# Optimization experiments

Hardware: AMD Instinct MI355X
Metric: run time of the kernel (lower is better)

Reference implementation:

```python
import jax, jax.numpy as jnp
import numpy as np


def fwht(x):
    """Fast Walsh-Hadamard transform along last axis (n must be a power of 2).
    Loop runs log2(n) times (fixed, ~12 iters) -- fully vectorized butterflies."""
    n = x.shape[-1]
    prefix = x.shape[:-1]
    x = x.reshape(-1, n)
    h = 1
    while h < n:
        x = x.reshape(-1, n // (2 * h), 2, h)
        a, b = x[:, :, 0, :], x[:, :, 1, :]
        x = jnp.stack([a + b, a - b], axis=2).reshape(-1, n)
        h *= 2
    return x.reshape(prefix + (n,))


def setup_inputs() -> dict:
    key = jax.random.key(0)
    ks = jax.random.split(key, 8)
    Bz, S, N, M = 4, 2048, 4096, 4096   # batch, seq, in_features, out_features
    CODESZ, CB_SIZE, RANK = 8, 256, 64
    inp = {}
    inp["input"] = jax.random.normal(ks[0], (Bz, S, N), dtype=jnp.float32)
    inp["Qidxs"] = jax.random.randint(ks[1], (M, N // CODESZ), 0, CB_SIZE, dtype=jnp.int32)
    inp["codebook_vals"] = jax.random.normal(ks[2], (CB_SIZE, CODESZ), dtype=jnp.float32)
    # SU/SV are random sign vectors in QuIP#
    inp["SU"] = jnp.sign(jax.random.normal(ks[3], (N,), dtype=jnp.float32))
    inp["SV"] = jnp.sign(jax.random.normal(ks[4], (M,), dtype=jnp.float32))
    inp["Wscale"] = jnp.ones((), dtype=jnp.float32)
    inp["A"] = jax.random.normal(ks[5], (M, RANK), dtype=jnp.float32) * 0.01
    inp["B"] = jax.random.normal(ks[6], (RANK, N), dtype=jnp.float32) * 0.01
    return inp


def reference(input, Qidxs, codebook_vals, SU, SV, Wscale, A, B):
    n = SU.shape[0]   # in_features
    m = SV.shape[0]   # out_features
    lead = input.shape[:-1]
    x = input.reshape(-1, n).astype(jnp.float32)          # [T, n]
    # input rotation: x <- H^T (x * SU) / sqrt(n)   (matmul_hadUt, K=1 case)
    x = fwht(x * SU) * (1.0 / jnp.sqrt(jnp.float32(n)))
    # low-rank correction branch (rank > 0)
    Bx = x @ B.T                                          # [T, rank]
    # dequantize: codebook lookup [m, n/codesz, codesz] -> [m, n]
    W = codebook_vals[Qidxs].reshape(m, n)
    z = (x @ W.T) * Wscale                                # [T, m]
    z = z + Bx @ A.T
    # output rotation: z <- SV * (H z) / sqrt(m)
    z = fwht(z) * (1.0 / jnp.sqrt(jnp.float32(m))) * SV
    return z.reshape(lead + (m,))
```

## Files before the change

### kernel.cpp

```cpp
#include <hip/hip_runtime.h>
#include <hip/hip_bf16.h>


typedef __attribute__((ext_vector_type(8))) short short8;
typedef __attribute__((ext_vector_type(4))) float f32x4;

#define T_ROWS 8192
#define NDIM   4096
#define MDIM   4096
#define NT     (NDIM / 64)

__device__ __forceinline__ void gld_lds16(const void* g, void* lds_uniform) {
    __builtin_amdgcn_global_load_lds(
        (const __attribute__((address_space(1))) unsigned int*)(unsigned long long)(uintptr_t)g,
        (__attribute__((address_space(3))) unsigned int*)(unsigned int)(uintptr_t)lds_uniform,
        16, 0, 0);
}

__device__ __forceinline__ void bfly(float& a, float& b) {
    float s = a + b, d = a - b; a = s; b = d;
}

__device__ __forceinline__ void fwht16(float* v) {
#pragma unroll
    for (int h = 1; h <= 8; h <<= 1)
#pragma unroll
        for (int j = 0; j < 16; ++j)
            if (!(j & h)) bfly(v[j], v[j | h]);
}

__global__ __launch_bounds__(256) void fwht_in_kernel(
        const float* __restrict__ in, const float* __restrict__ SU,
        __hip_bfloat16* __restrict__ xout) {
    __shared__ float sh[4352];
    const int t = threadIdx.x;
    const size_t r = blockIdx.x;
    float v[16];
    {
        const float4* s4 = (const float4*)(in + (r << 12) + t * 16);
        const float4* u4 = (const float4*)(SU + t * 16);
#pragma unroll
        for (int q = 0; q < 4; ++q) {
            float4 a = s4[q], u = u4[q];
            v[4 * q + 0] = a.x * u.x; v[4 * q + 1] = a.y * u.y;
            v[4 * q + 2] = a.z * u.z; v[4 * q + 3] = a.w * u.w;
        }
    }
    fwht16(v);
#pragma unroll
    for (int j = 0; j < 16; ++j) sh[17 * t + j] = v[j];
    __syncthreads();
    const int baseB = (t & 15) + 272 * (t >> 4);
#pragma unroll
    for (int j = 0; j < 16; ++j) v[j] = sh[baseB + 17 * j];
    fwht16(v);
#pragma unroll
    for (int j = 0; j < 16; ++j) sh[baseB + 17 * j] = v[j];
    __syncthreads();
    const int baseC = t + (t >> 4);
#pragma unroll
    for (int j = 0; j < 16; ++j) v[j] = sh[baseC + 272 * j];
    fwht16(v);
    __hip_bfloat16* dst = xout + (r << 12);
#pragma unroll
    for (int j = 0; j < 16; ++j)
        dst[(j << 8) + t] = __float2bfloat16(v[j] * 0.015625f);
}

__global__ __launch_bounds__(256) void fwht_out_kernel(
        float* __restrict__ z, const float* __restrict__ SV) {
    __shared__ float sh[4352];
    const int t = threadIdx.x;
    const size_t r = blockIdx.x;
    float* row = z + (r << 12);
    float v[16];
    {
        const float4* s4 = (const float4*)(row + t * 16);
#pragma unroll
        for (int q = 0; q < 4; ++q) {
            float4 a = s4[q];
            v[4 * q + 0] = a.x; v[4 * q + 1] = a.y;
            v[4 * q + 2] = a.z; v[4 * q + 3] = a.w;
        }
    }
    fwht16(v);
#pragma unroll
    for (int j = 0; j < 16; ++j) sh[17 * t + j] = v[j];
    __syncthreads();
    const int baseB = (t & 15) + 272 * (t >> 4);
#pragma unroll
    for (int j = 0; j < 16; ++j) v[j] = sh[baseB + 17 * j];
    fwht16(v);
#pragma unroll
    for (int j = 0; j < 16; ++j) sh[baseB + 17 * j] = v[j];
    __syncthreads();
    const int baseC = t + (t >> 4);
#pragma unroll
    for (int j = 0; j < 16; ++j) v[j] = sh[baseC + 272 * j];
    fwht16(v);
#pragma unroll
    for (int j = 0; j < 16; ++j)
        row[(j << 8) + t] = v[j] * 0.015625f * SV[(j << 8) + t];
}

__global__ __launch_bounds__(256) void dequant_kernel(
        const int* __restrict__ Qidxs, const float* __restrict__ cb,
        const float* __restrict__ Wscale, const float* __restrict__ A,
        const float* __restrict__ B, __hip_bfloat16* __restrict__ Weff) {
    __shared__ float At[64][68];
    __shared__ float Bs[64][68];
    __shared__ float cbs[2048];
    const int t = threadIdx.x;
    const int i0 = blockIdx.y * 64, j0 = blockIdx.x * 64;

    {
        const float* ga = A + (size_t)i0 * 64;
        const int r = t >> 2, kb = (t & 3) * 16;
#pragma unroll
        for (int j = 0; j < 16; ++j) At[kb + j][r] = ga[t * 16 + j];
        const int k = t >> 2, c0 = (t & 3) * 16;
        const float* gb = B + (size_t)k * NDIM + j0 + c0;
#pragma unroll
        for (int j = 0; j < 16; ++j) Bs[k][c0 + j] = gb[j];
#pragma unroll
        for (int j = 0; j < 8; ++j) cbs[t * 8 + j] = cb[t * 8 + j];
    }
    __syncthreads();

    const int ty = t >> 4, tx = t & 15;
    float acc[4][4];
#pragma unroll
    for (int a = 0; a < 4; ++a)
#pragma unroll
        for (int b = 0; b < 4; ++b) acc[a][b] = 0.f;

#pragma unroll 8
    for (int k = 0; k < 64; ++k) {
        const float4 av = *(const float4*)&At[k][ty * 4];
        const float4 bv = *(const float4*)&Bs[k][tx * 4];
        const float aa[4] = {av.x, av.y, av.z, av.w};
        const float bb[4] = {bv.x, bv.y, bv.z, bv.w};
#pragma unroll
        for (int ii = 0; ii < 4; ++ii)
#pragma unroll
            for (int jj = 0; jj < 4; ++jj) acc[ii][jj] += aa[ii] * bb[jj];
    }

    const float wsc = Wscale[0];
#pragma unroll
    for (int ii = 0; ii < 4; ++ii) {
        const int i = i0 + ty * 4 + ii;
        const int* qrow = Qidxs + (size_t)i * (NDIM / 8);
        union { __hip_bfloat16 h[4]; unsigned long long u; } pk;
#pragma unroll
        for (int jj = 0; jj < 4; ++jj) {
            const int j = j0 + tx * 4 + jj;
            const int idx = qrow[j >> 3];
            const float val = cbs[idx * 8 + (j & 7)] * wsc + acc[ii][jj];
            pk.h[jj] = __float2bfloat16(val);
        }
        *(unsigned long long*)&Weff[(size_t)i * NDIM + j0 + tx * 4] = pk.u;
    }
}

__global__ __launch_bounds__(512, 2) void gemm256_kernel(
        const __hip_bfloat16* __restrict__ X, const __hip_bfloat16* __restrict__ W,
        float* __restrict__ Z) {
    __shared__ short smem[65536];

    const int b = blockIdx.x;
    const int swz = (b & 7) * 64 + (b >> 3);
    const int bm = swz >> 4, bn = swz & 15;

    const int tid = threadIdx.x;
    const int lane = tid & 63, wid = tid >> 6;
    const int wm = wid >> 2, wn = wid & 3;
    const int lr = lane & 15, lk = lane >> 4;
    const int swb = (lr & 7) << 4;
    const int c0 = (((lk << 4)) ^ swb) >> 1;
    const int c1 = ((64 | (lk << 4)) ^ swb) >> 1;
    const int wbase = wid << 9;

    const int grow = tid >> 3;
    const int scol = (((tid & 7) ^ (grow & 7)) << 3);
    const __hip_bfloat16* gA = X + (size_t)(bm * 256 + grow) * NDIM + scol;
    const __hip_bfloat16* gB = W + (size_t)(bn * 256 + grow) * NDIM + scol;

#define STA2(OFS, H, Q, BUF) gld_lds16(gA + (size_t)(((H) * 128 + (Q) * 64) * NDIM) + (OFS), \
        &smem[(BUF) * 32768 + (H) * 8192 + (Q) * 4096 + wbase])
#define STB2(OFS, H, Q, BUF) gld_lds16(gB + (size_t)(((H) * 128 + (Q) * 64) * NDIM) + (OFS), \
        &smem[(BUF) * 32768 + 16384 + (H) * 8192 + (Q) * 4096 + wbase])
#define STAGE_A(OFS, BUF) do { STA2(OFS,0,0,BUF); STA2(OFS,0,1,BUF); \
                               STA2(OFS,1,0,BUF); STA2(OFS,1,1,BUF); } while (0)
#define STAGE_B(OFS, BUF) do { STB2(OFS,0,0,BUF); STB2(OFS,0,1,BUF); \
                               STB2(OFS,1,0,BUF); STB2(OFS,1,1,BUF); } while (0)

#define RDA(D0, D1, D2, D3, M0, AB) do { \
    D0 = *(const short8*)((AB) + ((M0) * 16 + lr) * 64 + c0); \
    D1 = *(const short8*)((AB) + ((M0) * 16 + lr) * 64 + c1); \
    D2 = *(const short8*)((AB) + ((M0) * 16 + 16 + lr) * 64 + c0); \
    D3 = *(const short8*)((AB) + ((M0) * 16 + 16 + lr) * 64 + c1); \
} while (0)

#define RDB(BARR, BUF) do { \
    const short* bB_ = smem + (BUF) * 32768 + 16384 + (wn * 64 + lr) * 64; \
    _Pragma("unroll") \
    for (int n = 0; n < 4; ++n) { \
        BARR[2 * n]     = *(const short8*)(bB_ + n * 1024 + c0); \
        BARR[2 * n + 1] = *(const short8*)(bB_ + n * 1024 + c1); \
    } \
} while (0)

#define MFMA2(A0, A1, E0, E1, M0, BF) do { \
    _Pragma("unroll") \
    for (int n = 0; n < 4; ++n) \
        acc[M0][n] = __builtin_amdgcn_mfma_f32_16x16x32_bf16(A0, BF[2 * n], acc[M0][n], 0, 0, 0); \
    _Pragma("unroll") \
    for (int n = 0; n < 4; ++n) \
        acc[(M0) + 1][n] = __builtin_amdgcn_mfma_f32_16x16x32_bf16(E0, BF[2 * n], acc[(M0) + 1][n], 0, 0, 0); \
    _Pragma("unroll") \
    for (int n = 0; n < 4; ++n) \
        acc[M0][n] = __builtin_amdgcn_mfma_f32_16x16x32_bf16(A1, BF[2 * n + 1], acc[M0][n], 0, 0, 0); \
    _Pragma("unroll") \
    for (int n = 0; n < 4; ++n) \
        acc[(M0) + 1][n] = __builtin_amdgcn_mfma_f32_16x16x32_bf16(E1, BF[2 * n + 1], acc[(M0) + 1][n], 0, 0, 0); \
} while (0)

#define TILE(CUR, BF, BN, DO_STA, DO_STB, DO_BN, LAST) do { \
    const short* aBase = smem + (CUR) * 32768 + wm * 8192; \
    if (DO_STA) STAGE_A(64, 1 - (CUR)); \
    if (DO_STB) STAGE_B(128, (CUR)); \
    RDA(xa0, xa1, xb0, xb1, 0, aBase); \
    RDA(ya0, ya1, yb0, yb1, 2, aBase); \
    MFMA2(xa0, xa1, xb0, xb1, 0, BF); \
    RDA(xa0, xa1, xb0, xb1, 4, aBase); \
    MFMA2(ya0, ya1, yb0, yb1, 2, BF); \
    RDA(ya0, ya1, yb0, yb1, 6, aBase); \
    if (DO_BN) RDB(BN, 1 - (CUR)); \
    MFMA2(xa0, xa1, xb0, xb1, 4, BF); \
    MFMA2(ya0, ya1, yb0, yb1, 6, BF); \
    if (!(LAST)) { \
        asm volatile("s_waitcnt lgkmcnt(0)" ::: "memory"); \
        asm volatile("s_waitcnt vmcnt(0)" ::: "memory"); \
        __builtin_amdgcn_s_barrier(); \
    } \
    gA += 64; gB += 64; \
} while (0)

    f32x4 acc[8][4];
#pragma unroll
    for (int m = 0; m < 8; ++m)
#pragma unroll
        for (int n = 0; n < 4; ++n) acc[m][n] = 0.f;

    short8 B0r[8], B1r[8];
    short8 xa0, xa1, xb0, xb1, ya0, ya1, yb0, yb1;

    STAGE_A(0, 0);
    STAGE_B(0, 0);
    STAGE_B(64, 1);
    asm volatile("s_waitcnt vmcnt(0)" ::: "memory");
    __builtin_amdgcn_s_barrier();
    RDB(B0r, 0);
    asm volatile("s_waitcnt lgkmcnt(0)" ::: "memory");
    __builtin_amdgcn_s_barrier();

    for (int i = 0; i < 31; ++i) {
        TILE(0, B0r, B1r, 1, 1, 1, 0);
        TILE(1, B1r, B0r, 1, 1, 1, 0);
    }
    TILE(0, B0r, B1r, 1, 0, 1, 0);
    TILE(1, B1r, B0r, 0, 0, 0, 1);

    const size_t r0 = (size_t)bm * 256 + wm * 128 + (lk << 2);
    const size_t cb0 = (size_t)bn * 256 + wn * 64 + lr;
#pragma unroll
    for (int m = 0; m < 8; ++m)
#pragma unroll
        for (int n = 0; n < 4; ++n) {
            const size_t col = cb0 + n * 16;
#pragma unroll
            for (int j = 0; j < 4; ++j)
                Z[(r0 + m * 16 + j) * MDIM + col] = acc[m][n][j];
        }
}

extern "C" void kernel_launch(void* const* d_in, const int* in_sizes, int n_in,
                              void* d_out, int out_size, void* d_ws, size_t ws_size,
                              hipStream_t stream) {
    const float* input  = (const float*)d_in[0];
    const int*   Qidxs  = (const int*)d_in[1];
    const float* cbvals = (const float*)d_in[2];
    const float* SU     = (const float*)d_in[3];
    const float* SV     = (const float*)d_in[4];
    const float* Wscale = (const float*)d_in[5];
    const float* A      = (const float*)d_in[6];
    const float* B      = (const float*)d_in[7];
    float* out = (float*)d_out;

    __hip_bfloat16* xbf = (__hip_bfloat16*)d_ws;
    __hip_bfloat16* wbf = (__hip_bfloat16*)((char*)d_ws + (size_t)T_ROWS * NDIM * 2);

    fwht_in_kernel<<<T_ROWS, 256, 0, stream>>>(input, SU, xbf);
    dequant_kernel<<<dim3(MDIM / 64, MDIM / 64), 256, 0, stream>>>(
        Qidxs, cbvals, Wscale, A, B, wbf);
    gemm256_kernel<<<(T_ROWS / 256) * (MDIM / 256), 512, 0, stream>>>(xbf, wbf, out);
    fwht_out_kernel<<<T_ROWS, 256, 0, stream>>>(out, SV);
}
```

Before: 356.9 us.

## Switch GEMM to 32x32x16 MFMA with rotating register pipeline

Replaces the 16x16x32 bf16 MFMA tiling with 32x32x16 MFMAs, so each wave keeps eight 32x32 accumulators and loads A and B fragments together per K-chunk. Fragment reads rotate through three register sets, and the next tile's first chunk is prefetched after the barrier, which staggers the wave's K-chunk order by wm to cut LDS bank conflicts. The B staging is now fully double-buffered alongside A instead of the earlier offset scheme. The goal is fewer LDS reads per FLOP and a higher MFMA issue rate. The cost is more register pressure and a more intricate schedule.

```diff
diff --git a/kernel.cpp b/kernel.cpp
--- a/kernel.cpp
+++ b/kernel.cpp
@@ -3,12 +3,11 @@
 
 
 typedef __attribute__((ext_vector_type(8))) short short8;
-typedef __attribute__((ext_vector_type(4))) float f32x4;
+typedef __attribute__((ext_vector_type(16))) float f32x16;
 
 #define T_ROWS 8192
 #define NDIM   4096
 #define MDIM   4096
-#define NT     (NDIM / 64)
 
 __device__ __forceinline__ void gld_lds16(const void* g, void* lds_uniform) {
     __builtin_amdgcn_global_load_lds(
@@ -175,10 +174,12 @@
     const int tid = threadIdx.x;
     const int lane = tid & 63, wid = tid >> 6;
     const int wm = wid >> 2, wn = wid & 3;
-    const int lr = lane & 15, lk = lane >> 4;
-    const int swb = (lr & 7) << 4;
-    const int c0 = (((lk << 4)) ^ swb) >> 1;
-    const int c1 = ((64 | (lk << 4)) ^ swb) >> 1;
+    const int l31 = lane & 31, kg = lane >> 5, le7 = lane & 7;
+    const int rowV = l31 * 64;
+    const int ck0 = ((2 * ((0 + 2 * wm) & 3) + kg) ^ le7) << 3;
+    const int ck1 = ((2 * ((1 + 2 * wm) & 3) + kg) ^ le7) << 3;
+    const int ck2 = ((2 * ((2 + 2 * wm) & 3) + kg) ^ le7) << 3;
+    const int ck3 = ((2 * ((3 + 2 * wm) & 3) + kg) ^ le7) << 3;
     const int wbase = wid << 9;
 
     const int grow = tid >> 3;
@@ -195,94 +196,88 @@
 #define STAGE_B(OFS, BUF) do { STB2(OFS,0,0,BUF); STB2(OFS,0,1,BUF); \
                                STB2(OFS,1,0,BUF); STB2(OFS,1,1,BUF); } while (0)
 
-#define RDA(D0, D1, D2, D3, M0, AB) do { \
-    D0 = *(const short8*)((AB) + ((M0) * 16 + lr) * 64 + c0); \
-    D1 = *(const short8*)((AB) + ((M0) * 16 + lr) * 64 + c1); \
-    D2 = *(const short8*)((AB) + ((M0) * 16 + 16 + lr) * 64 + c0); \
-    D3 = *(const short8*)((AB) + ((M0) * 16 + 16 + lr) * 64 + c1); \
+#define RD32_I(CK, BUF, A0,A1,A2,A3,B0,B1) do { \
+    const short* aP = smem + (BUF) * 32768 + wm * 8192 + rowV + (CK); \
+    const short* bP = smem + (BUF) * 32768 + 16384 + wn * 4096 + rowV + (CK); \
+    A0 = *(const short8*)(aP); \
+    A1 = *(const short8*)(aP + 2048); \
+    A2 = *(const short8*)(aP + 4096); \
+    A3 = *(const short8*)(aP + 6144); \
+    B0 = *(const short8*)(bP); \
+    B1 = *(const short8*)(bP + 2048); \
 } while (0)
-
-#define RDB(BARR, BUF) do { \
-    const short* bB_ = smem + (BUF) * 32768 + 16384 + (wn * 64 + lr) * 64; \
-    _Pragma("unroll") \
-    for (int n = 0; n < 4; ++n) { \
-        BARR[2 * n]     = *(const short8*)(bB_ + n * 1024 + c0); \
-        BARR[2 * n + 1] = *(const short8*)(bB_ + n * 1024 + c1); \
-    } \
+#define RD32(...) RD32_I(__VA_ARGS__)
+
+#define MM32_I(A0,A1,A2,A3,B0,B1) do { \
+    c00 = __builtin_amdgcn_mfma_f32_32x32x16_bf16(A0, B0, c00, 0, 0, 0); \
+    c10 = __builtin_amdgcn_mfma_f32_32x32x16_bf16(A1, B0, c10, 0, 0, 0); \
+    c01 = __builtin_amdgcn_mfma_f32_32x32x16_bf16(A0, B1, c01, 0, 0, 0); \
+    c11 = __builtin_amdgcn_mfma_f32_32x32x16_bf16(A1, B1, c11, 0, 0, 0); \
+    c20 = __builtin_amdgcn_mfma_f32_32x32x16_bf16(A2, B0, c20, 0, 0, 0); \
+    c30 = __builtin_amdgcn_mfma_f32_32x32x16_bf16(A3, B0, c30, 0, 0, 0); \
+    c21 = __builtin_amdgcn_mfma_f32_32x32x16_bf16(A2, B1, c21, 0, 0, 0); \
+    c31 = __builtin_amdgcn_mfma_f32_32x32x16_bf16(A3, B1, c31, 0, 0, 0); \
 } while (0)
-
-#define MFMA2(A0, A1, E0, E1, M0, BF) do { \
-    _Pragma("unroll") \
-    for (int n = 0; n < 4; ++n) \
-        acc[M0][n] = __builtin_amdgcn_mfma_f32_16x16x32_bf16(A0, BF[2 * n], acc[M0][n], 0, 0, 0); \
-    _Pragma("unroll") \
-    for (int n = 0; n < 4; ++n) \
-        acc[(M0) + 1][n] = __builtin_amdgcn_mfma_f32_16x16x32_bf16(E0, BF[2 * n], acc[(M0) + 1][n], 0, 0, 0); \
-    _Pragma("unroll") \
-    for (int n = 0; n < 4; ++n) \
-        acc[M0][n] = __builtin_amdgcn_mfma_f32_16x16x32_bf16(A1, BF[2 * n + 1], acc[M0][n], 0, 0, 0); \
-    _Pragma("unroll") \
-    for (int n = 0; n < 4; ++n) \
-        acc[(M0) + 1][n] = __builtin_amdgcn_mfma_f32_16x16x32_bf16(E1, BF[2 * n + 1], acc[(M0) + 1][n], 0, 0, 0); \
-} while (0)
-
-#define TILE(CUR, BF, BN, DO_STA, DO_STB, DO_BN, LAST) do { \
-    const short* aBase = smem + (CUR) * 32768 + wm * 8192; \
-    if (DO_STA) STAGE_A(64, 1 - (CUR)); \
-    if (DO_STB) STAGE_B(128, (CUR)); \
-    RDA(xa0, xa1, xb0, xb1, 0, aBase); \
-    RDA(ya0, ya1, yb0, yb1, 2, aBase); \
-    MFMA2(xa0, xa1, xb0, xb1, 0, BF); \
-    RDA(xa0, xa1, xb0, xb1, 4, aBase); \
-    MFMA2(ya0, ya1, yb0, yb1, 2, BF); \
-    RDA(ya0, ya1, yb0, yb1, 6, aBase); \
-    if (DO_BN) RDB(BN, 1 - (CUR)); \
-    MFMA2(xa0, xa1, xb0, xb1, 4, BF); \
-    MFMA2(ya0, ya1, yb0, yb1, 6, BF); \
+#define MM32(...) MM32_I(__VA_ARGS__)
+
+#define SARGS0 s0a0,s0a1,s0a2,s0a3,s0b0,s0b1
+#define SARGS1 s1a0,s1a1,s1a2,s1a3,s1b0,s1b1
+#define SARGS2 s2a0,s2a1,s2a2,s2a3,s2b0,s2b1
+
+#define TILE32_I(CUR, M3P, DO_ST, DO_PF, LAST, \
+               SA0,SA1,SA2,SA3,SA4,SA5, SB0,SB1,SB2,SB3,SB4,SB5, \
+               SC0,SC1,SC2,SC3,SC4,SC5) do { \
+    if (DO_ST) { STAGE_A(64, 1 - (CUR)); STAGE_B(64, 1 - (CUR)); } \
+    if (M3P) MM32(SA0,SA1,SA2,SA3,SA4,SA5);              \
+    RD32(ck1, CUR, SC0,SC1,SC2,SC3,SC4,SC5); \
+    MM32(SB0,SB1,SB2,SB3,SB4,SB5);                       \
+    RD32(ck2, CUR, SA0,SA1,SA2,SA3,SA4,SA5); \
+    MM32(SC0,SC1,SC2,SC3,SC4,SC5);                       \
+    RD32(ck3, CUR, SB0,SB1,SB2,SB3,SB4,SB5); \
+    MM32(SA0,SA1,SA2,SA3,SA4,SA5);                       \
     if (!(LAST)) { \
         asm volatile("s_waitcnt lgkmcnt(0)" ::: "memory"); \
         asm volatile("s_waitcnt vmcnt(0)" ::: "memory"); \
         __builtin_amdgcn_s_barrier(); \
+        asm volatile("" ::: "memory"); \
     } \
+    if (DO_PF) RD32(ck0, 1 - (CUR), SA0,SA1,SA2,SA3,SA4,SA5);   \
     gA += 64; gB += 64; \
 } while (0)
-
-    f32x4 acc[8][4];
-#pragma unroll
-    for (int m = 0; m < 8; ++m)
-#pragma unroll
-        for (int n = 0; n < 4; ++n) acc[m][n] = 0.f;
-
-    short8 B0r[8], B1r[8];
-    short8 xa0, xa1, xb0, xb1, ya0, ya1, yb0, yb1;
+#define TILE32(...) TILE32_I(__VA_ARGS__)
+
+    f32x16 c00 = {0}, c01 = {0}, c10 = {0}, c11 = {0};
+    f32x16 c20 = {0}, c21 = {0}, c30 = {0}, c31 = {0};
+    short8 s0a0, s0a1, s0a2, s0a3, s0b0, s0b1;
+    short8 s1a0, s1a1, s1a2, s1a3, s1b0, s1b1;
+    short8 s2a0, s2a1, s2a2, s2a3, s2b0, s2b1;
 
     STAGE_A(0, 0);
     STAGE_B(0, 0);
-    STAGE_B(64, 1);
     asm volatile("s_waitcnt vmcnt(0)" ::: "memory");
     __builtin_amdgcn_s_barrier();
-    RDB(B0r, 0);
-    asm volatile("s_waitcnt lgkmcnt(0)" ::: "memory");
-    __builtin_amdgcn_s_barrier();
-
+    asm volatile("" ::: "memory");
+    RD32(ck0, 0, SARGS1);
+
+    TILE32(0, 0, 1, 1, 0, SARGS0, SARGS1, SARGS2);
     for (int i = 0; i < 31; ++i) {
-        TILE(0, B0r, B1r, 1, 1, 1, 0);
-        TILE(1, B1r, B0r, 1, 1, 1, 0);
-    }
-    TILE(0, B0r, B1r, 1, 0, 1, 0);
-    TILE(1, B1r, B0r, 0, 0, 0, 1);
-
-    const size_t r0 = (size_t)bm * 256 + wm * 128 + (lk << 2);
-    const size_t cb0 = (size_t)bn * 256 + wn * 64 + lr;
-#pragma unroll
-    for (int m = 0; m < 8; ++m)
-#pragma unroll
-        for (int n = 0; n < 4; ++n) {
-            const size_t col = cb0 + n * 16;
-#pragma unroll
-            for (int j = 0; j < 4; ++j)
-                Z[(r0 + m * 16 + j) * MDIM + col] = acc[m][n][j];
-        }
+        TILE32(1, 1, 1, 1, 0, SARGS1, SARGS0, SARGS2);
+        TILE32(0, 1, 1, 1, 0, SARGS0, SARGS1, SARGS2);
+    }
+    TILE32(1, 1, 0, 0, 1, SARGS1, SARGS0, SARGS2);
+    MM32(SARGS0);
+
+    const size_t r0 = (size_t)bm * 256 + wm * 128 + 4 * (lane >> 5);
+    const size_t cb0 = (size_t)bn * 256 + wn * 64 + l31;
+#define CWR(CC, M, N) do { \
+    _Pragma("unroll") \
+    for (int rg = 0; rg < 16; ++rg) \
+        Z[(r0 + (M) * 32 + (rg & 3) + 8 * (rg >> 2)) * MDIM + cb0 + (N) * 32] = CC[rg]; \
+} while (0)
+    CWR(c00, 0, 0); CWR(c01, 0, 1);
+    CWR(c10, 1, 0); CWR(c11, 1, 1);
+    CWR(c20, 2, 0); CWR(c21, 2, 1);
+    CWR(c30, 3, 0); CWR(c31, 3, 1);
 }
 
 extern "C" void kernel_launch(void* const* d_in, const int* in_sizes, int n_in,
```

Measured after the change: 381.3 us. 1.07x slower.
